# Performance work log

Hardware: AMD Instinct MI355X
Metric: run time of the kernel (lower is better)

## Reference

```python
import jax, jax.numpy as jnp
import numpy as np

IN_DIM = 512
RATIO = 8
QK_DIM = IN_DIM // RATIO  # 64
B, C, H, W = 8, IN_DIM, 64, 64


def setup_inputs() -> dict:
    key = jax.random.key(0)
    ks = jax.random.split(key, 9)
    x = jax.random.normal(ks[0], (B, C, H, W), dtype=jnp.float32)
    y = jax.random.normal(ks[1], (B, C, H, W), dtype=jnp.float32)
    z = jax.random.normal(ks[2], (B, C, H, W), dtype=jnp.float32)
    # 1x1 conv weights, xavier_normal with gain=0.02: std = gain*sqrt(2/(fan_in+fan_out))
    def xavier(k, out_c, in_c, gain=0.02):
        std = gain * np.sqrt(2.0 / (in_c + out_c))
        return jax.random.normal(k, (out_c, in_c), dtype=jnp.float32) * std
    Wq = xavier(ks[3], QK_DIM, C)
    Wk = xavier(ks[4], QK_DIM, C)
    Wv = xavier(ks[5], C, C)
    bq = jnp.zeros((QK_DIM,), dtype=jnp.float32)
    bk = jnp.zeros((QK_DIM,), dtype=jnp.float32)
    bv = jnp.zeros((C,), dtype=jnp.float32)
    gamma = jnp.zeros((1,), dtype=jnp.float32)
    return {"x": x, "y": y, "z": z, "Wq": Wq, "bq": bq, "Wk": Wk,
            "bk": bk, "Wv": Wv, "bv": bv, "gamma": gamma}


def reference(x, y, z, Wq, bq, Wk, bk, Wv, bv, gamma):
    b, c, h, w = x.shape
    n = h * w
    # 1x1 convs == per-pixel linear projections
    q = (jnp.einsum('oc,bchw->bohw', Wq, x) + bq[None, :, None, None]).reshape(b, -1, n)  # [B, d, N]
    k = (jnp.einsum('oc,bchw->bohw', Wk, y) + bk[None, :, None, None]).reshape(b, -1, n)  # [B, d, N]
    v = (jnp.einsum('oc,bchw->bohw', Wv, z) + bv[None, :, None, None]).reshape(b, -1, n)  # [B, C, N]
    # energy[b, i, j] = <q[:, i], k[:, j]>, no scaling (matches original)
    energy = jnp.einsum('bdn,bdm->bnm', q, k)      # [B, N, N]
    attention = jax.nn.softmax(energy, axis=-1)     # softmax over keys
    # out = value @ attention^T : out[:, c, i] = sum_j v[:, c, j] * attention[:, i, j]
    out = jnp.einsum('bcj,bij->bci', v, attention)  # [B, C, N]
    out = out.reshape(b, c, h, w)
    out = gamma[0] * out + x
    return out
```

## Files before the change

kernel.cpp:

```cpp
#include <hip/hip_runtime.h>
#include <hip/hip_bf16.h>
#include <hip/hip_fp8.h>
#include <stdint.h>

#define B_   8
#define C_   512
#define NPIX 4096
#define VLDB 4160

typedef __attribute__((ext_vector_type(8))) short bf16x8;
typedef __attribute__((ext_vector_type(4))) float f32x4;

__device__ __forceinline__ uint16_t f2bf(float f) {
    union { float f; uint32_t u; } v; v.f = f;
    uint32_t u = v.u;
    return (uint16_t)((u + 0x7FFFu + ((u >> 16) & 1u)) >> 16);
}

__device__ __forceinline__ uint32_t pk2(float a, float b) {
    union { __hip_bfloat162 h; uint32_t u; } c;
    c.h = __float22bfloat162_rn(make_float2(a, b));
    return c.u;
}

__device__ __forceinline__ float fexp2(float x) {
#if __has_builtin(__builtin_amdgcn_exp2f)
    return __builtin_amdgcn_exp2f(x);
#else
    return exp2f(x);
#endif
}

template<bool HI>
__device__ __forceinline__ uint32_t pk_fp8(float a, float b, uint32_t old) {
#if __has_builtin(__builtin_amdgcn_cvt_pk_fp8_f32)
    return __builtin_amdgcn_cvt_pk_fp8_f32(a, b, old, HI);
#else
    union { __hip_fp8_storage_t s[4]; uint32_t u; } r; r.u = old;
    r.s[HI * 2 + 0] = __hip_cvt_float_to_fp8(a, __HIP_SATFINITE, __HIP_E4M3);
    r.s[HI * 2 + 1] = __hip_cvt_float_to_fp8(b, __HIP_SATFINITE, __HIP_E4M3);
    return r.u;
#endif
}
__device__ __forceinline__ uint8_t f2fp8(float a) {
#if __has_builtin(__builtin_amdgcn_cvt_pk_fp8_f32)
    uint32_t u = __builtin_amdgcn_cvt_pk_fp8_f32(a, 0.f, 0u, false);
    return (uint8_t)(u & 0xFF);
#else
    return __hip_cvt_float_to_fp8(a, __HIP_SATFINITE, __HIP_E4M3);
#endif
}

__global__ __launch_bounds__(256, 2) void proj_kernel(
    const float* __restrict__ X, const float* __restrict__ W,
    const float* __restrict__ bias, uint16_t* __restrict__ out,
    float scale)
{
    __shared__ char xt[64 * 128];
    const int b  = blockIdx.z;
    const int n0 = blockIdx.x * 64;
    const int t = threadIdx.x, w = t >> 6, l = t & 63;
    const int l15 = l & 15, lg = l >> 4;
    const float* Xb = X + (size_t)b * C_ * NPIX + n0;

    f32x4 acc[4] = {};

    for (int cc = 0; cc < C_; cc += 64) {
        __syncthreads();
        #pragma unroll
        for (int i = 0; i < 16; i += 2) {
            int c = w * 16 + i;
            float f0 = Xb[(size_t)(cc + c) * NPIX + l];
            float f1 = Xb[(size_t)(cc + c + 1) * NPIX + l];
            uint32_t pair = pk2(f0, f1);
            int byte = (l * 128 + c * 2) ^ ((l & 7) << 4);
            *(uint32_t*)(xt + byte) = pair;
        }
        __syncthreads();
        #pragma unroll
        for (int kk = 0; kk < 2; kk++) {
            int o  = w * 16 + l15;
            int cb = cc + kk * 32 + lg * 8;
            float4 wa = *(const float4*)&W[(size_t)o * C_ + cb];
            float4 wb = *(const float4*)&W[(size_t)o * C_ + cb + 4];
            union { bf16x8 v; uint32_t u[4]; } afu;
            afu.u[0] = pk2(wa.x, wa.y); afu.u[1] = pk2(wa.z, wa.w);
            afu.u[2] = pk2(wb.x, wb.y); afu.u[3] = pk2(wb.z, wb.w);
            #pragma unroll
            for (int jt = 0; jt < 4; jt++) {
                int n = jt * 16 + l15;
                int byte = (n * 128 + (kk * 32 + lg * 8) * 2) ^ ((n & 7) << 4);
                bf16x8 bfr = *(bf16x8*)(xt + byte);
                acc[jt] = __builtin_amdgcn_mfma_f32_16x16x32_bf16(afu.v, bfr, acc[jt], 0, 0, 0);
            }
        }
    }
    int og = w * 16 + lg * 4;
    #pragma unroll
    for (int jt = 0; jt < 4; jt++) {
        int n = n0 + jt * 16 + l15;
        #pragma unroll
        for (int r = 0; r < 4; r++) {
            float v = (acc[jt][r] + bias[og + r]) * scale;
            out[((size_t)b * NPIX + n) * 64 + og + r] = f2bf(v);
        }
    }
}

__global__ __launch_bounds__(256, 2) void projv_kernel(
    const float* __restrict__ X, const float* __restrict__ W,
    const float* __restrict__ bias, uint8_t* __restrict__ outp)
{
    __shared__ char xt[64 * 1024];
    const int b  = blockIdx.z;
    const int n0 = blockIdx.x * 64;
    const int t = threadIdx.x, w = t >> 6, l = t & 63;
    const int l15 = l & 15, lg = l >> 4;
    const float* Xb = X + (size_t)b * C_ * NPIX + n0;

    for (int cc = 0; cc < C_; cc += 64) {
        #pragma unroll
        for (int i = 0; i < 16; i += 2) {
            int c = cc + w * 16 + i;
            float f0 = Xb[(size_t)c * NPIX + l];
            float f1 = Xb[(size_t)(c + 1) * NPIX + l];
            uint32_t pair = pk2(f0, f1);
            int byte = (l * 1024 + c * 2) ^ ((l & 7) << 4);
            *(uint32_t*)(xt + byte) = pair;
        }
    }
    __syncthreads();

    #pragma unroll 1
    for (int o0 = 0; o0 < C_; o0 += 64) {
        f32x4 acc[4] = {};
        #pragma unroll 1
        for (int cc = 0; cc < C_; cc += 64) {
            #pragma unroll
            for (int kk = 0; kk < 2; kk++) {
                int o  = o0 + w * 16 + l15;
                int cb = cc + kk * 32 + lg * 8;
                float4 wa = *(const float4*)&W[(size_t)o * C_ + cb];
                float4 wb = *(const float4*)&W[(size_t)o * C_ + cb + 4];
                union { bf16x8 v; uint32_t u[4]; } afu;
                afu.u[0] = pk2(wa.x, wa.y); afu.u[1] = pk2(wa.z, wa.w);
                afu.u[2] = pk2(wb.x, wb.y); afu.u[3] = pk2(wb.z, wb.w);
                #pragma unroll
                for (int jt = 0; jt < 4; jt++) {
                    int n = jt * 16 + l15;
                    int byte = (n * 1024 + cb * 2) ^ ((n & 7) << 4);
                    bf16x8 bfr = *(bf16x8*)(xt + byte);
                    acc[jt] = __builtin_amdgcn_mfma_f32_16x16x32_bf16(afu.v, bfr, acc[jt], 0, 0, 0);
                }
            }
        }
        int og = o0 + w * 16 + lg * 4;
        #pragma unroll
        for (int jt = 0; jt < 4; jt++) {
            int j6 = jt * 16 + l15;
            int pos = ((j6 >> 3) & 3) * 16 + ((j6 >> 5) << 3) + (j6 & 7);
            #pragma unroll
            for (int r = 0; r < 4; r++) {
                float v = (acc[jt][r] + bias[og + r]) * 64.0f;
                outp[((size_t)b * C_ + og + r) * (size_t)VLDB + (size_t)(n0 >> 6) * 64 + pos] = f2fp8(v);
            }
        }
    }
}

__global__ __launch_bounds__(512, 1) void attn_kernel(
    const uint16_t* __restrict__ qT, const uint16_t* __restrict__ kT,
    const uint8_t* __restrict__ vB, const float* __restrict__ X,
    const float* __restrict__ gamma_p, float* __restrict__ out)
{
    __shared__ char  Pl[3][64 * 128];
    __shared__ float lsum[64][9];

    const int id = blockIdx.x;
    const int b  = id & 7;
    const int qt = id >> 3;
    const int i0 = qt * 64;

    const int t = threadIdx.x, w = t >> 6, l = t & 63;
    const int l15 = l & 15, lg = l >> 4;
    const int c0 = w * 64;

    auto barrier_lds = [&]() {
        asm volatile("s_waitcnt lgkmcnt(0)" ::: "memory");
        __builtin_amdgcn_s_barrier();
    };

    bf16x8 q8[4][2];
    #pragma unroll
    for (int it = 0; it < 4; it++)
        #pragma unroll
        for (int kk = 0; kk < 2; kk++)
            q8[it][kk] = *(const bf16x8*)&qT[((size_t)b * NPIX + i0 + it*16 + l15) * 64 + kk*32 + lg*8];

    f32x4 oacc[4][4] = {};
    float l_part[4] = {0.f, 0.f, 0.f, 0.f};

    const uint16_t* kTb = kT + (size_t)b * NPIX * 64;
    const uint8_t*  vBb = vB + ((size_t)b * C_ + c0) * (size_t)VLDB + lg * 16;
    const uint16_t* kROW = kTb + (size_t)(w * 16 + l15) * 64 + lg * 8;

    int vrowB[4];
    #pragma unroll
    for (int ct = 0; ct < 4; ct++) vrowB[ct] = (ct * 16 + l15) * VLDB;

    bf16x8 k8[2];
    ulong2 vreg[8];
    f32x4 s[4];

    auto loadK = [&](int step) {
        const uint16_t* p = kROW + (size_t)step * (128 * 64);
        k8[0] = *(const bf16x8*)p;
        k8[1] = *(const bf16x8*)(p + 32);
    };
    auto loadV = [&](int step) {
        const uint8_t* p = vBb + (size_t)step * 128;
        #pragma unroll
        for (int jh = 0; jh < 2; jh++)
            #pragma unroll
            for (int ct = 0; ct < 4; ct++)
                vreg[jh*4+ct] = *(const ulong2*)(p + vrowB[ct] + jh * 64);
    };
    auto QK = [&]() {
        #pragma unroll
        for (int it = 0; it < 4; it++) s[it] = f32x4{0.f, 0.f, 0.f, 0.f};
        __builtin_amdgcn_s_setprio(1);
        #pragma unroll
        for (int kk = 0; kk < 2; kk++)
            #pragma unroll
            for (int it = 0; it < 4; it++)
                s[it] = __builtin_amdgcn_mfma_f32_16x16x32_bf16(k8[kk], q8[it][kk], s[it], 0, 0, 0);
        __builtin_amdgcn_s_setprio(0);
    };
    auto PcomputeWrite = [&](char* Pn) {
        #pragma unroll
        for (int it = 0; it < 4; it++) {
            float e0 = fexp2(fminf(s[it][0], 60.f));
            float e1 = fexp2(fminf(s[it][1], 60.f));
            float e2 = fexp2(fminf(s[it][2], 60.f));
            float e3 = fexp2(fminf(s[it][3], 60.f));
            l_part[it] += (e0 + e1) + (e2 + e3);
            uint32_t p4 = pk_fp8<false>(e0, e1, 0u);
            p4 = pk_fp8<true>(e2, e3, p4);
            int i = it * 16 + l15;
            int byte = (i * 128 + w * 16 + lg * 4) ^ ((i & 15) << 3);
            *(uint32_t*)(Pn + byte) = p4;
        }
    };
    auto PV = [&](const char* P) {
        __builtin_amdgcn_s_setprio(1);
        #pragma unroll
        for (int jh = 0; jh < 2; jh++)
            #pragma unroll
            for (int kk = 0; kk < 2; kk++) {
                long pb[4];
                #pragma unroll
                for (int it = 0; it < 4; it++) {
                    int i = it * 16 + l15;
                    int byte = (i * 128 + jh * 64 + kk * 32 + lg * 8) ^ ((i & 15) << 3);
                    pb[it] = *(const long*)(P + byte);
                }
                #pragma unroll
                for (int ct = 0; ct < 4; ct++) {
                    long v8 = (long)(kk ? vreg[jh*4+ct].y : vreg[jh*4+ct].x);
                    #pragma unroll
                    for (int it = 0; it < 4; it++)
                        oacc[ct][it] = __builtin_amdgcn_mfma_f32_16x16x32_fp8_fp8(v8, pb[it], oacc[ct][it], 0, 0, 0);
                }
            }
        __builtin_amdgcn_s_setprio(0);
    };

    loadK(0);
    loadV(0);
    QK();
    loadK(1);
    PcomputeWrite(Pl[0]);
    QK();
    loadK(2);
    PcomputeWrite(Pl[1]);

    char* Pprev = Pl[0];
    char* Pcur  = Pl[1];
    char* Pnext = Pl[2];

    #pragma unroll 1
    for (int jt_ = 1; jt_ < 32; ++jt_) {
        barrier_lds();
        PV(Pprev);
        loadV(jt_);
        if (jt_ < 31) {
            QK();
            if (jt_ < 30) loadK(jt_ + 2);
            PcomputeWrite(Pnext);
        }
        char* tmp = Pprev; Pprev = Pcur; Pcur = Pnext; Pnext = tmp;
    }
    barrier_lds();
    PV(Pprev);

    #pragma unroll
    for (int it = 0; it < 4; it++) {
        float v = l_part[it];
        v += __shfl_xor(v, 16);
        v += __shfl_xor(v, 32);
        if (lg == 0) lsum[it * 16 + l15][w] = v;
    }
    __syncthreads();

    float gamma = gamma_p[0];
    float rl[4];
    #pragma unroll
    for (int it = 0; it < 4; it++) {
        int i = it * 16 + l15;
        float lt = ((lsum[i][0] + lsum[i][1]) + (lsum[i][2] + lsum[i][3]))
                 + ((lsum[i][4] + lsum[i][5]) + (lsum[i][6] + lsum[i][7]));
        rl[it] = 1.0f / (64.0f * lt);
    }
    #pragma unroll
    for (int ct = 0; ct < 4; ct++)
        #pragma unroll
        for (int r = 0; r < 4; r++) {
            int c = c0 + ct * 16 + lg * 4 + r;
            #pragma unroll
            for (int it = 0; it < 4; it++) {
                int n = i0 + it * 16 + l15;
                size_t idx = ((size_t)b * C_ + c) * NPIX + n;
                out[idx] = gamma * (oacc[ct][it][r] * rl[it]) + X[idx];
            }
        }
}

extern "C" void kernel_launch(void* const* d_in, const int* in_sizes, int n_in,
                              void* d_out, int out_size, void* d_ws, size_t ws_size,
                              hipStream_t stream) {
    const float* x     = (const float*)d_in[0];
    const float* y     = (const float*)d_in[1];
    const float* z     = (const float*)d_in[2];
    const float* Wq    = (const float*)d_in[3];
    const float* bq    = (const float*)d_in[4];
    const float* Wk    = (const float*)d_in[5];
    const float* bk    = (const float*)d_in[6];
    const float* Wv    = (const float*)d_in[7];
    const float* bv    = (const float*)d_in[8];
    const float* gamma = (const float*)d_in[9];
    float* out = (float*)d_out;

    uint16_t* qT = (uint16_t*)d_ws;
    uint16_t* kT = qT + (size_t)B_ * NPIX * 64;
    uint8_t*  vb = (uint8_t*)(kT + (size_t)B_ * NPIX * 64);

    proj_kernel <<<dim3(64, 1, 8), dim3(256), 0, stream>>>(x, Wq, bq, qT, 1.4426950408889634f);
    proj_kernel <<<dim3(64, 1, 8), dim3(256), 0, stream>>>(y, Wk, bk, kT, 1.0f);
    projv_kernel<<<dim3(64, 1, 8), dim3(256), 0, stream>>>(z, Wv, bv, vb);
    attn_kernel <<<dim3(512), dim3(512), 0, stream>>>(qT, kT, vb, x, gamma, out);
}
```

Measured before the change: 269.3 us.

## Pre-convert Wv to bf16 and process two pixel tiles per V-projection block

A new small kernel converts the value-projection weights to bf16 once per call, so the V projection no longer reloads fp32 weights and repacks them in its inner loop. Each projv block now stages two 64-pixel tiles of z in shared memory (128 KB) and reuses every weight fragment across both tiles. The grid is halved to 256 blocks. In exchange, occupancy drops to one block per CU, there is an extra kernel launch, and more accumulator registers are live.

```diff
diff --git a/kernel.cpp b/kernel.cpp
--- a/kernel.cpp
+++ b/kernel.cpp
@@ -49,6 +49,22 @@
 #else
     return __hip_cvt_float_to_fp8(a, __HIP_SATFINITE, __HIP_E4M3);
 #endif
+}
+
+__device__ __forceinline__ int perm64(int d) {
+    return ((d >> 3) & 3) * 16 + ((d >> 5) << 3) + (d & 7);
+}
+
+__global__ __launch_bounds__(256, 4) void convw_kernel(
+    const float* __restrict__ W, uint16_t* __restrict__ Wb)
+{
+    int i = (blockIdx.x * 256 + threadIdx.x) * 8;
+    float4 a = *(const float4*)&W[i];
+    float4 b = *(const float4*)&W[i + 4];
+    union { bf16x8 v; uint32_t u[4]; } r;
+    r.u[0] = pk2(a.x, a.y); r.u[1] = pk2(a.z, a.w);
+    r.u[2] = pk2(b.x, b.y); r.u[3] = pk2(b.z, b.w);
+    *(bf16x8*)&Wb[i] = r.v;
 }
 
 __global__ __launch_bounds__(256, 2) void proj_kernel(
@@ -107,62 +123,67 @@
     }
 }
 
-__global__ __launch_bounds__(256, 2) void projv_kernel(
-    const float* __restrict__ X, const float* __restrict__ W,
+__global__ __launch_bounds__(256, 1) void projv_kernel(
+    const float* __restrict__ X, const uint16_t* __restrict__ Wb,
     const float* __restrict__ bias, uint8_t* __restrict__ outp)
 {
-    __shared__ char xt[64 * 1024];
+    __shared__ char xt[2][64 * 1024];
     const int b  = blockIdx.z;
-    const int n0 = blockIdx.x * 64;
+    const int ng = blockIdx.x;
     const int t = threadIdx.x, w = t >> 6, l = t & 63;
     const int l15 = l & 15, lg = l >> 4;
-    const float* Xb = X + (size_t)b * C_ * NPIX + n0;
-
-    for (int cc = 0; cc < C_; cc += 64) {
-        #pragma unroll
-        for (int i = 0; i < 16; i += 2) {
-            int c = cc + w * 16 + i;
-            float f0 = Xb[(size_t)c * NPIX + l];
-            float f1 = Xb[(size_t)(c + 1) * NPIX + l];
-            uint32_t pair = pk2(f0, f1);
-            int byte = (l * 1024 + c * 2) ^ ((l & 7) << 4);
-            *(uint32_t*)(xt + byte) = pair;
+
+    #pragma unroll
+    for (int nt = 0; nt < 2; nt++) {
+        const float* Xb = X + (size_t)b * C_ * NPIX + (ng * 2 + nt) * 64;
+        for (int cc = 0; cc < C_; cc += 64) {
+            #pragma unroll
+            for (int i = 0; i < 16; i += 2) {
+                int c = cc + w * 16 + i;
+                float f0 = Xb[(size_t)c * NPIX + l];
+                float f1 = Xb[(size_t)(c + 1) * NPIX + l];
+                uint32_t pair = pk2(f0, f1);
+                int byte = (l * 1024 + c * 2) ^ ((l & 7) << 4);
+                *(uint32_t*)(xt[nt] + byte) = pair;
+            }
         }
     }
     __syncthreads();
 
     #pragma unroll 1
     for (int o0 = 0; o0 < C_; o0 += 64) {
-        f32x4 acc[4] = {};
+        f32x4 acc[2][4] = {};
         #pragma unroll 1
         for (int cc = 0; cc < C_; cc += 64) {
             #pragma unroll
             for (int kk = 0; kk < 2; kk++) {
                 int o  = o0 + w * 16 + l15;
                 int cb = cc + kk * 32 + lg * 8;
-                float4 wa = *(const float4*)&W[(size_t)o * C_ + cb];
-                float4 wb = *(const float4*)&W[(size_t)o * C_ + cb + 4];
-                union { bf16x8 v; uint32_t u[4]; } afu;
-                afu.u[0] = pk2(wa.x, wa.y); afu.u[1] = pk2(wa.z, wa.w);
-                afu.u[2] = pk2(wb.x, wb.y); afu.u[3] = pk2(wb.z, wb.w);
+                bf16x8 af = *(const bf16x8*)&Wb[(size_t)o * C_ + cb];
                 #pragma unroll
-                for (int jt = 0; jt < 4; jt++) {
-                    int n = jt * 16 + l15;
-                    int byte = (n * 1024 + cb * 2) ^ ((n & 7) << 4);
-                    bf16x8 bfr = *(bf16x8*)(xt + byte);
-                    acc[jt] = __builtin_amdgcn_mfma_f32_16x16x32_bf16(afu.v, bfr, acc[jt], 0, 0, 0);
+                for (int nt = 0; nt < 2; nt++)
+                    #pragma unroll
+                    for (int jt = 0; jt < 4; jt++) {
+                        int n = jt * 16 + l15;
+                        int byte = (n * 1024 + cb * 2) ^ ((n & 7) << 4);
+                        bf16x8 bfr = *(bf16x8*)(xt[nt] + byte);
+                        acc[nt][jt] = __builtin_amdgcn_mfma_f32_16x16x32_bf16(af, bfr, acc[nt][jt], 0, 0, 0);
+                    }
+            }
+        }
+        int og = o0 + w * 16 + lg * 4;
+        #pragma unroll
+        for (int nt = 0; nt < 2; nt++) {
+            int n0 = (ng * 2 + nt) * 64;
+            #pragma unroll
+            for (int jt = 0; jt < 4; jt++) {
+                int j6 = jt * 16 + l15;
+                int pos = perm64(j6);
+                #pragma unroll
+                for (int r = 0; r < 4; r++) {
+                    float v = (acc[nt][jt][r] + bias[og + r]) * 64.0f;
+                    outp[((size_t)b * C_ + og + r) * (size_t)VLDB + (size_t)(n0 >> 6) * 64 + pos] = f2fp8(v);
                 }
-            }
-        }
-        int og = o0 + w * 16 + lg * 4;
-        #pragma unroll
-        for (int jt = 0; jt < 4; jt++) {
-            int j6 = jt * 16 + l15;
-            int pos = ((j6 >> 3) & 3) * 16 + ((j6 >> 5) << 3) + (j6 & 7);
-            #pragma unroll
-            for (int r = 0; r < 4; r++) {
-                float v = (acc[jt][r] + bias[og + r]) * 64.0f;
-                outp[((size_t)b * C_ + og + r) * (size_t)VLDB + (size_t)(n0 >> 6) * 64 + pos] = f2fp8(v);
             }
         }
     }
@@ -350,12 +371,14 @@
     const float* gamma = (const float*)d_in[9];
     float* out = (float*)d_out;
 
-    uint16_t* qT = (uint16_t*)d_ws;
-    uint16_t* kT = qT + (size_t)B_ * NPIX * 64;
-    uint8_t*  vb = (uint8_t*)(kT + (size_t)B_ * NPIX * 64);
-
+    uint16_t* qT  = (uint16_t*)d_ws;
+    uint16_t* kT  = qT + (size_t)B_ * NPIX * 64;
+    uint8_t*  vb  = (uint8_t*)(kT + (size_t)B_ * NPIX * 64);
+    uint16_t* Wvb = (uint16_t*)(vb + (size_t)B_ * C_ * VLDB);
+
+    convw_kernel<<<dim3(128), dim3(256), 0, stream>>>(Wv, Wvb);
     proj_kernel <<<dim3(64, 1, 8), dim3(256), 0, stream>>>(x, Wq, bq, qT, 1.4426950408889634f);
     proj_kernel <<<dim3(64, 1, 8), dim3(256), 0, stream>>>(y, Wk, bk, kT, 1.0f);
-    projv_kernel<<<dim3(64, 1, 8), dim3(256), 0, stream>>>(z, Wv, bv, vb);
+    projv_kernel<<<dim3(32, 1, 8), dim3(256), 0, stream>>>(z, Wvb, bv, vb);
     attn_kernel <<<dim3(512), dim3(512), 0, stream>>>(qT, kT, vb, x, gamma, out);
 }
```

Result: faster. 257.6 us (-4.4%).
